# Optimization experiments

Hardware: AMD Instinct MI355X
Metric: run time of the kernel (lower is better)

## Reference

```python
import jax, jax.numpy as jnp
import numpy as np

N = 50000   # nodes
E = 800000  # edges (avg degree 16)
D = 256     # input = hidden = output dim
L = 3       # num_layers


def setup_inputs() -> dict:
    key = jax.random.key(0)
    k0, k1, k2, k3 = jax.random.split(key, 4)
    x = jax.random.normal(k0, (N, D), dtype=jnp.float32)
    edge_index = jax.random.randint(k1, (2, E), 0, N, dtype=jnp.int32)
    # SAGEConv params per layer: lin_l (neighbor path, with bias), lin_r (root path)
    Wl = jax.random.normal(k2, (L, D, D), dtype=jnp.float32) * 0.05
    Wr = jax.random.normal(k3, (L, D, D), dtype=jnp.float32) * 0.05
    b = jnp.zeros((L, D), dtype=jnp.float32)
    return {"x": x, "edge_index": edge_index, "Wl": Wl, "Wr": Wr, "b": b}


def reference(x, edge_index, Wl, Wr, b):
    src = edge_index[0]
    dst = edge_index[1]
    # in-degree for mean aggregation (clamped to avoid div-by-zero)
    deg = jax.ops.segment_sum(jnp.ones((E,), x.dtype), dst, num_segments=N)
    inv_deg = (1.0 / jnp.maximum(deg, 1.0))[:, None]  # [N,1]
    h = x
    for i in range(L):
        # gather source features, scatter-add into destinations, then mean
        agg = jax.ops.segment_sum(h[src], dst, num_segments=N) * inv_deg  # [N,D]
        h = agg @ Wl[i] + h @ Wr[i] + b[i]
        if i < L - 1:
            h = jax.nn.relu(h)  # dropout(p=0.1) is identity in eval mode
    return h
```

## Files before the change

kernel.cpp:

```cpp
#include <hip/hip_runtime.h>


typedef __attribute__((ext_vector_type(8))) _Float16 f16x8;
typedef __attribute__((ext_vector_type(4))) float f32x4;

__global__ void count_deg_kernel(const int* __restrict__ dst,
                                 int* __restrict__ deg, int E) {
    int e = blockIdx.x * blockDim.x + threadIdx.x;
    if (e < E) atomicAdd(&deg[dst[e]], 1);
}

__device__ __forceinline__ int block_excl_scan_256(int v, int tid) {
    int lane = tid & 63, w = tid >> 6;
    int x = v;
#pragma unroll
    for (int off = 1; off < 64; off <<= 1) {
        int y = __shfl_up(x, off);
        if (lane >= off) x += y;
    }
    __shared__ int wsum[4], woff[4];
    if (lane == 63) wsum[w] = x;
    __syncthreads();
    if (tid == 0) {
        int a = 0;
#pragma unroll
        for (int i = 0; i < 4; ++i) { woff[i] = a; a += wsum[i]; }
    }
    __syncthreads();
    return woff[w] + x - v;
}

__global__ void scan_phase1(const int* __restrict__ deg,
                            int* __restrict__ partial, int n) {
    int base = blockIdx.x * 1024;
    int s = 0;
    for (int i = threadIdx.x; i < 1024; i += 256) {
        int idx = base + i;
        s += (idx < n) ? deg[idx] : 0;
    }
    __shared__ int ws4[4];
    int lane = threadIdx.x & 63, w = threadIdx.x >> 6;
#pragma unroll
    for (int off = 32; off; off >>= 1) s += __shfl_down(s, off);
    if (lane == 0) ws4[w] = s;
    __syncthreads();
    if (threadIdx.x == 0)
        partial[blockIdx.x] = ws4[0] + ws4[1] + ws4[2] + ws4[3];
}

__global__ void scan_phase2(int* __restrict__ partial, int nb,
                            int* __restrict__ rowptr, int n, int E) {
    int tid = threadIdx.x;
    int v = (tid < nb) ? partial[tid] : 0;
    int ex = block_excl_scan_256(v, tid);
    if (tid < nb) partial[tid] = ex;
    if (tid == 0) rowptr[n] = E;
}

__global__ void scan_phase3(const int* __restrict__ deg,
                            const int* __restrict__ partial,
                            int* __restrict__ rowptr, int* __restrict__ cursor,
                            float* __restrict__ inv_deg, int n) {
    int base = blockIdx.x * 1024 + threadIdx.x * 4;
    int d[4];
#pragma unroll
    for (int j = 0; j < 4; ++j) {
        int idx = base + j;
        d[j] = (idx < n) ? deg[idx] : 0;
    }
    int tsum = d[0] + d[1] + d[2] + d[3];
    int ex = block_excl_scan_256(tsum, threadIdx.x);
    int run = partial[blockIdx.x] + ex;
#pragma unroll
    for (int j = 0; j < 4; ++j) {
        int idx = base + j;
        if (idx < n) {
            rowptr[idx] = run;
            cursor[idx] = run;
            inv_deg[idx] = 1.0f / (float)max(d[j], 1);
        }
        run += d[j];
    }
}

__global__ void fill_csr_kernel(const int* __restrict__ src,
                                const int* __restrict__ dst,
                                int* __restrict__ cursor,
                                int* __restrict__ csr_src, int E) {
    int e = blockIdx.x * blockDim.x + threadIdx.x;
    if (e < E) {
        int d = dst[e];
        int pos = atomicAdd(&cursor[d], 1);
        csr_src[pos] = src[e];
    }
}

__global__ void presplit_w_kernel(const float* __restrict__ Wl,
                                  const float* __restrict__ Wr,
                                  _Float16* __restrict__ Wf, int total) {
    int idx = blockIdx.x * blockDim.x + threadIdx.x;
    if (idx >= total) return;
    int l = idx >> 17;
    int rem = idx & 131071;
    int s = rem >> 16;
    int kc = rem & 65535;
    int k = kc >> 8, c = kc & 255;
    const float* W = s ? Wr : Wl;
    float w = W[((size_t)l * 256 + k) * 256 + c];
    int k0c = k >> 5, g = (k >> 3) & 3, j = k & 7;
    int tile = c >> 4, col = c & 15;
    int fi = (l * 2 + s) * 65536 + k0c * 8192 + ((tile * 4 + g) * 16 + col) * 8 + j;
    Wf[fi] = (_Float16)w;
}

__device__ __forceinline__ void gemm_from_lds64(
    const _Float16 (*Ah)[65][8], int tid, const _Float16* __restrict__ Wf_l,
    const float* __restrict__ bias, _Float16* __restrict__ zl,
    _Float16* __restrict__ zr, int r0, int M) {
    const int wave = tid >> 6, lane = tid & 63;
    const int l15 = lane & 15, lg = lane >> 4;
    const int wr = (wave & 1) * 32;
    const int wc = (wave >> 1) * 64;

    f32x4 accl[2][4], accr[2][4];
#pragma unroll
    for (int rt = 0; rt < 2; ++rt)
#pragma unroll
        for (int t = 0; t < 4; ++t) {
            accl[rt][t] = (f32x4)(0.0f);
            accr[rt][t] = (f32x4)(0.0f);
        }

#pragma unroll
    for (int k0 = 0; k0 < 256; k0 += 32) {
        f16x8 a0 = *(const f16x8*)&Ah[(k0 >> 3) + lg][wr + l15][0];
        f16x8 a1 = *(const f16x8*)&Ah[(k0 >> 3) + lg][wr + 16 + l15][0];
        const _Float16* wb = Wf_l + (k0 >> 5) * 8192 + (lg * 16 + l15) * 8;
#pragma unroll
        for (int t = 0; t < 4; ++t) {
            int tg = (wc >> 4) + t;
            f16x8 bl = *(const f16x8*)&wb[tg * 512];
            f16x8 br = *(const f16x8*)&wb[65536 + tg * 512];
            accl[0][t] = __builtin_amdgcn_mfma_f32_16x16x32_f16(a0, bl,
                                                                accl[0][t], 0, 0, 0);
            accl[1][t] = __builtin_amdgcn_mfma_f32_16x16x32_f16(a1, bl,
                                                                accl[1][t], 0, 0, 0);
            accr[0][t] = __builtin_amdgcn_mfma_f32_16x16x32_f16(a0, br,
                                                                accr[0][t], 0, 0, 0);
            accr[1][t] = __builtin_amdgcn_mfma_f32_16x16x32_f16(a1, br,
                                                                accr[1][t], 0, 0, 0);
        }
    }

    float bv[4];
#pragma unroll
    for (int t = 0; t < 4; ++t) bv[t] = bias[wc + t * 16 + l15];
#pragma unroll
    for (int rt = 0; rt < 2; ++rt) {
#pragma unroll
        for (int r = 0; r < 4; ++r) {
            int grow = r0 + wr + rt * 16 + lg * 4 + r;
            if (grow >= M) continue;
#pragma unroll
            for (int t = 0; t < 4; ++t) {
                int col = wc + t * 16 + l15;
                zl[(size_t)grow * 256 + col] = (_Float16)accl[rt][t][r];
                zr[(size_t)grow * 256 + col] =
                    (_Float16)(accr[rt][t][r] + bv[t]);
            }
        }
    }
}

__device__ __forceinline__ void gemm_from_lds32(
    const _Float16 (*Ah)[33][8], int tid, const _Float16* __restrict__ Wf_l,
    const float* __restrict__ bias, _Float16* __restrict__ zl,
    _Float16* __restrict__ zr, int r0, int M) {
    const int wave = tid >> 6, lane = tid & 63;
    const int l15 = lane & 15, lg = lane >> 4;
    const int wr = (wave & 1) * 16;
    const int wc = (wave >> 1) * 64;

    f32x4 accl[4], accr[4];
#pragma unroll
    for (int t = 0; t < 4; ++t) {
        accl[t] = (f32x4)(0.0f);
        accr[t] = (f32x4)(0.0f);
    }

#pragma unroll
    for (int k0 = 0; k0 < 256; k0 += 32) {
        f16x8 a = *(const f16x8*)&Ah[(k0 >> 3) + lg][wr + l15][0];
        const _Float16* wb = Wf_l + (k0 >> 5) * 8192 + (lg * 16 + l15) * 8;
#pragma unroll
        for (int t = 0; t < 4; ++t) {
            int tg = (wc >> 4) + t;
            f16x8 bl = *(const f16x8*)&wb[tg * 512];
            f16x8 br = *(const f16x8*)&wb[65536 + tg * 512];
            accl[t] = __builtin_amdgcn_mfma_f32_16x16x32_f16(a, bl, accl[t],
                                                             0, 0, 0);
            accr[t] = __builtin_amdgcn_mfma_f32_16x16x32_f16(a, br, accr[t],
                                                             0, 0, 0);
        }
    }

    float bv[4];
#pragma unroll
    for (int t = 0; t < 4; ++t) bv[t] = bias[wc + t * 16 + l15];
#pragma unroll
    for (int r = 0; r < 4; ++r) {
        int grow = r0 + wr + lg * 4 + r;
        if (grow >= M) continue;
#pragma unroll
        for (int t = 0; t < 4; ++t) {
            int col = wc + t * 16 + l15;
            zl[(size_t)grow * 256 + col] = (_Float16)accl[t][r];
            zr[(size_t)grow * 256 + col] = (_Float16)(accr[t][r] + bv[t]);
        }
    }
}

__global__ __launch_bounds__(512) void gemm0_kernel(
    const float* __restrict__ xsrc, _Float16* __restrict__ zl,
    _Float16* __restrict__ zr, const _Float16* __restrict__ Wf_l,
    const float* __restrict__ bias, int M) {
    __shared__ __align__(16) _Float16 Ah[32][65][8];
    const int tid = threadIdx.x;
    const int r0 = blockIdx.x * 64;
#pragma unroll
    for (int i = 0; i < 4; ++i) {
        int idx = i * 512 + tid;
        int row = idx >> 5, g = idx & 31;
        int grow = r0 + row;
        f16x8 v = (f16x8)(_Float16)0;
        if (grow < M) {
            const float4* p = (const float4*)&xsrc[(size_t)grow * 256 + g * 8];
            float4 v0 = p[0], v1 = p[1];
            v[0] = (_Float16)v0.x; v[1] = (_Float16)v0.y;
            v[2] = (_Float16)v0.z; v[3] = (_Float16)v0.w;
            v[4] = (_Float16)v1.x; v[5] = (_Float16)v1.y;
            v[6] = (_Float16)v1.z; v[7] = (_Float16)v1.w;
        }
        *(f16x8*)&Ah[g][row][0] = v;
    }
    __syncthreads();
    gemm_from_lds64(Ah, tid, Wf_l, bias, zl, zr, r0, M);
}

__global__ __launch_bounds__(512) void fused_layer_kernel(
    const _Float16* __restrict__ zl_in, const _Float16* __restrict__ zr_in,
    _Float16* __restrict__ zl_out, _Float16* __restrict__ zr_out,
    const int* __restrict__ rowptr, const int* __restrict__ csr_src,
    const float* __restrict__ inv_deg, const _Float16* __restrict__ Wf_l,
    const float* __restrict__ bias, int M) {
    __shared__ __align__(16) _Float16 Ah[32][33][8];
    const int tid = threadIdx.x;
    const int hw = tid >> 5, li = tid & 31;
    const int r0 = blockIdx.x * 32;

#pragma unroll
    for (int i = 0; i < 2; ++i) {
        int row = hw * 2 + i;
        int v = r0 + row;
        f16x8 hv = (f16x8)(_Float16)0;
        if (v < M) {
            int beg = rowptr[v], end = rowptr[v + 1];
            float acc[8] = {0.f, 0.f, 0.f, 0.f, 0.f, 0.f, 0.f, 0.f};
            for (int e = beg; e < end; e += 8) {
                f16x8 t[8];
#pragma unroll
                for (int k = 0; k < 8; ++k) {
                    int ee = min(e + k, end - 1);
                    int u = csr_src[ee];
                    t[k] = *(const f16x8*)&zl_in[(size_t)u * 256 + li * 8];
                }
#pragma unroll
                for (int k = 0; k < 8; ++k) {
                    if (e + k < end) {
#pragma unroll
                        for (int j = 0; j < 8; ++j) acc[j] += (float)t[k][j];
                    }
                }
            }
            float sc = inv_deg[v];
            f16x8 zp = *(const f16x8*)&zr_in[(size_t)v * 256 + li * 8];
#pragma unroll
            for (int j = 0; j < 8; ++j)
                hv[j] = (_Float16)fmaxf(acc[j] * sc + (float)zp[j], 0.0f);
        }
        *(f16x8*)&Ah[li][row][0] = hv;
    }
    __syncthreads();
    gemm_from_lds32(Ah, tid, Wf_l, bias, zl_out, zr_out, r0, M);
}

__global__ void combine_final_kernel(const _Float16* __restrict__ zl,
                                     const _Float16* __restrict__ zr,
                                     const int* __restrict__ rowptr,
                                     const int* __restrict__ csr_src,
                                     const float* __restrict__ inv_deg,
                                     float* __restrict__ fout, int n) {
    int hw = threadIdx.x >> 5, li = threadIdx.x & 31;
    int v = blockIdx.x * 8 + hw;
    if (v >= n) return;
    int beg = rowptr[v], end = rowptr[v + 1];
    float acc[8] = {0.f, 0.f, 0.f, 0.f, 0.f, 0.f, 0.f, 0.f};
    for (int e = beg; e < end; e += 8) {
        f16x8 t[8];
#pragma unroll
        for (int k = 0; k < 8; ++k) {
            int ee = min(e + k, end - 1);
            int u = csr_src[ee];
            t[k] = *(const f16x8*)&zl[(size_t)u * 256 + li * 8];
        }
#pragma unroll
        for (int k = 0; k < 8; ++k) {
            if (e + k < end) {
#pragma unroll
                for (int j = 0; j < 8; ++j) acc[j] += (float)t[k][j];
            }
        }
    }
    float sc = inv_deg[v];
    f16x8 zp = *(const f16x8*)&zr[(size_t)v * 256 + li * 8];
    float o[8];
#pragma unroll
    for (int j = 0; j < 8; ++j) o[j] = acc[j] * sc + (float)zp[j];
    float4* op = (float4*)&fout[(size_t)v * 256 + li * 8];
    op[0] = make_float4(o[0], o[1], o[2], o[3]);
    op[1] = make_float4(o[4], o[5], o[6], o[7]);
}

extern "C" void kernel_launch(void* const* d_in, const int* in_sizes, int n_in,
                              void* d_out, int out_size, void* d_ws, size_t ws_size,
                              hipStream_t stream) {
    const int D = 256;
    const int N = in_sizes[0] / D;
    const int E = in_sizes[1] / 2;
    const int L = in_sizes[2] / (D * D);

    const float* x  = (const float*)d_in[0];
    const int*   ei = (const int*)d_in[1];
    const float* Wl = (const float*)d_in[2];
    const float* Wr = (const float*)d_in[3];
    const float* b  = (const float*)d_in[4];
    const int* src = ei;
    const int* dst = ei + E;

    size_t off = 0;
    auto alloc = [&](size_t bytes) {
        void* p = (char*)d_ws + off;
        off += (bytes + 255) & ~(size_t)255;
        return p;
    };
    int*   deg     = (int*)alloc((size_t)N * 4);
    int*   rowptr  = (int*)alloc((size_t)(N + 1) * 4);
    int*   cursor  = (int*)alloc((size_t)N * 4);
    float* inv_deg = (float*)alloc((size_t)N * 4);
    int*   csr_src = (int*)alloc((size_t)E * 4);
    int*   partial = (int*)alloc(256 * 4);
    _Float16* zlA = (_Float16*)alloc((size_t)N * D * 2);
    _Float16* zrA = (_Float16*)alloc((size_t)N * D * 2);
    _Float16* Wf  = (_Float16*)alloc((size_t)L * 2 * 65536 * 2);
    (void)ws_size;

    _Float16* zlB = (_Float16*)d_out;
    _Float16* zrB = zlB + (size_t)N * D;
    float* outf = (float*)d_out;

    const int scan_blocks = (N + 1023) / 1024;

    hipMemsetAsync(deg, 0, (size_t)N * 4, stream);
    hipLaunchKernelGGL(count_deg_kernel, dim3((E + 255) / 256), dim3(256), 0,
                       stream, dst, deg, E);
    hipLaunchKernelGGL(scan_phase1, dim3(scan_blocks), dim3(256), 0, stream,
                       deg, partial, N);
    hipLaunchKernelGGL(scan_phase2, dim3(1), dim3(256), 0, stream,
                       partial, scan_blocks, rowptr, N, E);
    hipLaunchKernelGGL(scan_phase3, dim3(scan_blocks), dim3(256), 0, stream,
                       deg, partial, rowptr, cursor, inv_deg, N);
    hipLaunchKernelGGL(fill_csr_kernel, dim3((E + 255) / 256), dim3(256), 0,
                       stream, src, dst, cursor, csr_src, E);

    int wtotal = L * 2 * 65536;
    hipLaunchKernelGGL(presplit_w_kernel, dim3((wtotal + 255) / 256), dim3(256),
                       0, stream, Wl, Wr, Wf, wtotal);

    const int gemm0_blocks = (N + 63) / 64;
    const int fused_blocks = (N + 31) / 32;
    const int comb_blocks = (N + 7) / 8;

    hipLaunchKernelGGL(gemm0_kernel, dim3(gemm0_blocks), dim3(512), 0, stream,
                       x, zlA, zrA, Wf, b, N);
    hipLaunchKernelGGL(fused_layer_kernel, dim3(fused_blocks), dim3(512), 0,
                       stream, zlA, zrA, zlB, zrB, rowptr, csr_src, inv_deg,
                       Wf + 131072, b + D, N);
    hipLaunchKernelGGL(fused_layer_kernel, dim3(fused_blocks), dim3(512), 0,
                       stream, zlB, zrB, zlA, zrA, rowptr, csr_src, inv_deg,
                       Wf + 262144, b + 2 * D, N);
    hipLaunchKernelGGL(combine_final_kernel, dim3(comb_blocks), dim3(256), 0,
                       stream, zlA, zrA, rowptr, csr_src, inv_deg, outf, N);
}
```

Before: 389.6 us.

## Widen fused layer tiles, prefetch weights, merge memset, vectorize CSR build

The fused aggregation+GEMM layer now handles 64 rows per block instead of 32 and reuses the 64-row GEMM routine, so each block reads the weights once for twice as many rows. The GEMM inner loop now loads the next K-slice of weights into registers while the current slice's MFMAs run. The degree memset is folded into the weight presplit kernel, which now launches first. Degree counting and CSR fill each handle two edges per thread with int2 loads. The 64-row tile halves the number of blocks in the gather-heavy layers, which may reduce latency hiding, and the register double buffer raises register pressure.

```diff
diff --git a/kernel.cpp b/kernel.cpp
--- a/kernel.cpp
+++ b/kernel.cpp
@@ -6,8 +6,14 @@
 
 __global__ void count_deg_kernel(const int* __restrict__ dst,
                                  int* __restrict__ deg, int E) {
-    int e = blockIdx.x * blockDim.x + threadIdx.x;
-    if (e < E) atomicAdd(&deg[dst[e]], 1);
+    int i = (blockIdx.x * blockDim.x + threadIdx.x) * 2;
+    if (i + 1 < E) {
+        int2 d = *(const int2*)&dst[i];
+        atomicAdd(&deg[d.x], 1);
+        atomicAdd(&deg[d.y], 1);
+    } else if (i < E) {
+        atomicAdd(&deg[dst[i]], 1);
+    }
 }
 
 __device__ __forceinline__ int block_excl_scan_256(int v, int tid) {
@@ -87,18 +93,26 @@
                                 const int* __restrict__ dst,
                                 int* __restrict__ cursor,
                                 int* __restrict__ csr_src, int E) {
-    int e = blockIdx.x * blockDim.x + threadIdx.x;
-    if (e < E) {
-        int d = dst[e];
-        int pos = atomicAdd(&cursor[d], 1);
-        csr_src[pos] = src[e];
+    int i = (blockIdx.x * blockDim.x + threadIdx.x) * 2;
+    if (i + 1 < E) {
+        int2 d = *(const int2*)&dst[i];
+        int2 s = *(const int2*)&src[i];
+        int p0 = atomicAdd(&cursor[d.x], 1);
+        csr_src[p0] = s.x;
+        int p1 = atomicAdd(&cursor[d.y], 1);
+        csr_src[p1] = s.y;
+    } else if (i < E) {
+        int p = atomicAdd(&cursor[dst[i]], 1);
+        csr_src[p] = src[i];
     }
 }
 
 __global__ void presplit_w_kernel(const float* __restrict__ Wl,
                                   const float* __restrict__ Wr,
-                                  _Float16* __restrict__ Wf, int total) {
+                                  _Float16* __restrict__ Wf,
+                                  int* __restrict__ deg, int N, int total) {
     int idx = blockIdx.x * blockDim.x + threadIdx.x;
+    if (idx < N) deg[idx] = 0;
     if (idx >= total) return;
     int l = idx >> 17;
     int rem = idx & 131071;
@@ -121,6 +135,8 @@
     const int l15 = lane & 15, lg = lane >> 4;
     const int wr = (wave & 1) * 32;
     const int wc = (wave >> 1) * 64;
+    const int tg0 = wc >> 4;
+    const _Float16* wbase = Wf_l + (lg * 16 + l15) * 8;
 
     f32x4 accl[2][4], accr[2][4];
 #pragma unroll
@@ -131,24 +147,43 @@
             accr[rt][t] = (f32x4)(0.0f);
         }
 
-#pragma unroll
-    for (int k0 = 0; k0 < 256; k0 += 32) {
-        f16x8 a0 = *(const f16x8*)&Ah[(k0 >> 3) + lg][wr + l15][0];
-        f16x8 a1 = *(const f16x8*)&Ah[(k0 >> 3) + lg][wr + 16 + l15][0];
-        const _Float16* wb = Wf_l + (k0 >> 5) * 8192 + (lg * 16 + l15) * 8;
+    f16x8 blc[4], brc[4];
+#pragma unroll
+    for (int t = 0; t < 4; ++t) {
+        blc[t] = *(const f16x8*)&wbase[(tg0 + t) * 512];
+        brc[t] = *(const f16x8*)&wbase[65536 + (tg0 + t) * 512];
+    }
+
+#pragma unroll
+    for (int s = 0; s < 8; ++s) {
+        f16x8 bln[4], brn[4];
+        if (s < 7) {
+            const _Float16* wn = wbase + (s + 1) * 8192;
+#pragma unroll
+            for (int t = 0; t < 4; ++t) {
+                bln[t] = *(const f16x8*)&wn[(tg0 + t) * 512];
+                brn[t] = *(const f16x8*)&wn[65536 + (tg0 + t) * 512];
+            }
+        }
+        f16x8 a0 = *(const f16x8*)&Ah[s * 4 + lg][wr + l15][0];
+        f16x8 a1 = *(const f16x8*)&Ah[s * 4 + lg][wr + 16 + l15][0];
 #pragma unroll
         for (int t = 0; t < 4; ++t) {
-            int tg = (wc >> 4) + t;
-            f16x8 bl = *(const f16x8*)&wb[tg * 512];
-            f16x8 br = *(const f16x8*)&wb[65536 + tg * 512];
-            accl[0][t] = __builtin_amdgcn_mfma_f32_16x16x32_f16(a0, bl,
+            accl[0][t] = __builtin_amdgcn_mfma_f32_16x16x32_f16(a0, blc[t],
                                                                 accl[0][t], 0, 0, 0);
-            accl[1][t] = __builtin_amdgcn_mfma_f32_16x16x32_f16(a1, bl,
+            accl[1][t] = __builtin_amdgcn_mfma_f32_16x16x32_f16(a1, blc[t],
                                                                 accl[1][t], 0, 0, 0);
-            accr[0][t] = __builtin_amdgcn_mfma_f32_16x16x32_f16(a0, br,
+            accr[0][t] = __builtin_amdgcn_mfma_f32_16x16x32_f16(a0, brc[t],
                                                                 accr[0][t], 0, 0, 0);
-            accr[1][t] = __builtin_amdgcn_mfma_f32_16x16x32_f16(a1, br,
+            accr[1][t] = __builtin_amdgcn_mfma_f32_16x16x32_f16(a1, brc[t],
                                                                 accr[1][t], 0, 0, 0);
+        }
+        if (s < 7) {
+#pragma unroll
+            for (int t = 0; t < 4; ++t) {
+                blc[t] = bln[t];
+                brc[t] = brn[t];
+            }
         }
     }
 
@@ -168,54 +203,6 @@
                 zr[(size_t)grow * 256 + col] =
                     (_Float16)(accr[rt][t][r] + bv[t]);
             }
-        }
-    }
-}
-
-__device__ __forceinline__ void gemm_from_lds32(
-    const _Float16 (*Ah)[33][8], int tid, const _Float16* __restrict__ Wf_l,
-    const float* __restrict__ bias, _Float16* __restrict__ zl,
-    _Float16* __restrict__ zr, int r0, int M) {
-    const int wave = tid >> 6, lane = tid & 63;
-    const int l15 = lane & 15, lg = lane >> 4;
-    const int wr = (wave & 1) * 16;
-    const int wc = (wave >> 1) * 64;
-
-    f32x4 accl[4], accr[4];
-#pragma unroll
-    for (int t = 0; t < 4; ++t) {
-        accl[t] = (f32x4)(0.0f);
-        accr[t] = (f32x4)(0.0f);
-    }
-
-#pragma unroll
-    for (int k0 = 0; k0 < 256; k0 += 32) {
-        f16x8 a = *(const f16x8*)&Ah[(k0 >> 3) + lg][wr + l15][0];
-        const _Float16* wb = Wf_l + (k0 >> 5) * 8192 + (lg * 16 + l15) * 8;
-#pragma unroll
-        for (int t = 0; t < 4; ++t) {
-            int tg = (wc >> 4) + t;
-            f16x8 bl = *(const f16x8*)&wb[tg * 512];
-            f16x8 br = *(const f16x8*)&wb[65536 + tg * 512];
-            accl[t] = __builtin_amdgcn_mfma_f32_16x16x32_f16(a, bl, accl[t],
-                                                             0, 0, 0);
-            accr[t] = __builtin_amdgcn_mfma_f32_16x16x32_f16(a, br, accr[t],
-                                                             0, 0, 0);
-        }
-    }
-
-    float bv[4];
-#pragma unroll
-    for (int t = 0; t < 4; ++t) bv[t] = bias[wc + t * 16 + l15];
-#pragma unroll
-    for (int r = 0; r < 4; ++r) {
-        int grow = r0 + wr + lg * 4 + r;
-        if (grow >= M) continue;
-#pragma unroll
-        for (int t = 0; t < 4; ++t) {
-            int col = wc + t * 16 + l15;
-            zl[(size_t)grow * 256 + col] = (_Float16)accl[t][r];
-            zr[(size_t)grow * 256 + col] = (_Float16)(accr[t][r] + bv[t]);
         }
     }
 }
@@ -253,18 +240,20 @@
     const int* __restrict__ rowptr, const int* __restrict__ csr_src,
     const float* __restrict__ inv_deg, const _Float16* __restrict__ Wf_l,
     const float* __restrict__ bias, int M) {
-    __shared__ __align__(16) _Float16 Ah[32][33][8];
+    __shared__ __align__(16) _Float16 Ah[32][65][8];
     const int tid = threadIdx.x;
     const int hw = tid >> 5, li = tid & 31;
-    const int r0 = blockIdx.x * 32;
-
-#pragma unroll
-    for (int i = 0; i < 2; ++i) {
-        int row = hw * 2 + i;
+    const int r0 = blockIdx.x * 64;
+
+#pragma unroll
+    for (int i = 0; i < 4; ++i) {
+        int row = hw * 4 + i;
         int v = r0 + row;
         f16x8 hv = (f16x8)(_Float16)0;
         if (v < M) {
             int beg = rowptr[v], end = rowptr[v + 1];
+            float sc = inv_deg[v];
+            f16x8 zp = *(const f16x8*)&zr_in[(size_t)v * 256 + li * 8];
             float acc[8] = {0.f, 0.f, 0.f, 0.f, 0.f, 0.f, 0.f, 0.f};
             for (int e = beg; e < end; e += 8) {
                 f16x8 t[8];
@@ -282,8 +271,6 @@
                     }
                 }
             }
-            float sc = inv_deg[v];
-            f16x8 zp = *(const f16x8*)&zr_in[(size_t)v * 256 + li * 8];
 #pragma unroll
             for (int j = 0; j < 8; ++j)
                 hv[j] = (_Float16)fmaxf(acc[j] * sc + (float)zp[j], 0.0f);
@@ -291,7 +278,7 @@
         *(f16x8*)&Ah[li][row][0] = hv;
     }
     __syncthreads();
-    gemm_from_lds32(Ah, tid, Wf_l, bias, zl_out, zr_out, r0, M);
+    gemm_from_lds64(Ah, tid, Wf_l, bias, zl_out, zr_out, r0, M);
 }
 
 __global__ void combine_final_kernel(const _Float16* __restrict__ zl,
@@ -370,32 +357,30 @@
 
     const int scan_blocks = (N + 1023) / 1024;
 
-    hipMemsetAsync(deg, 0, (size_t)N * 4, stream);
-    hipLaunchKernelGGL(count_deg_kernel, dim3((E + 255) / 256), dim3(256), 0,
-                       stream, dst, deg, E);
+    int wtotal = L * 2 * 65536;
+    hipLaunchKernelGGL(presplit_w_kernel, dim3((wtotal + 255) / 256), dim3(256),
+                       0, stream, Wl, Wr, Wf, deg, N, wtotal);
+
+    hipLaunchKernelGGL(count_deg_kernel, dim3((E / 2 + 255) / 256), dim3(256),
+                       0, stream, dst, deg, E);
     hipLaunchKernelGGL(scan_phase1, dim3(scan_blocks), dim3(256), 0, stream,
                        deg, partial, N);
     hipLaunchKernelGGL(scan_phase2, dim3(1), dim3(256), 0, stream,
                        partial, scan_blocks, rowptr, N, E);
     hipLaunchKernelGGL(scan_phase3, dim3(scan_blocks), dim3(256), 0, stream,
                        deg, partial, rowptr, cursor, inv_deg, N);
-    hipLaunchKernelGGL(fill_csr_kernel, dim3((E + 255) / 256), dim3(256), 0,
-                       stream, src, dst, cursor, csr_src, E);
-
-    int wtotal = L * 2 * 65536;
-    hipLaunchKernelGGL(presplit_w_kernel, dim3((wtotal + 255) / 256), dim3(256),
-                       0, stream, Wl, Wr, Wf, wtotal);
-
-    const int gemm0_blocks = (N + 63) / 64;
-    const int fused_blocks = (N + 31) / 32;
+    hipLaunchKernelGGL(fill_csr_kernel, dim3((E / 2 + 255) / 256), dim3(256),
+                       0, stream, src, dst, cursor, csr_src, E);
+
+    const int gemm_blocks = (N + 63) / 64;
     const int comb_blocks = (N + 7) / 8;
 
-    hipLaunchKernelGGL(gemm0_kernel, dim3(gemm0_blocks), dim3(512), 0, stream,
+    hipLaunchKernelGGL(gemm0_kernel, dim3(gemm_blocks), dim3(512), 0, stream,
                        x, zlA, zrA, Wf, b, N);
-    hipLaunchKernelGGL(fused_layer_kernel, dim3(fused_blocks), dim3(512), 0,
+    hipLaunchKernelGGL(fused_layer_kernel, dim3(gemm_blocks), dim3(512), 0,
                        stream, zlA, zrA, zlB, zrB, rowptr, csr_src, inv_deg,
                        Wf + 131072, b + D, N);
-    hipLaunchKernelGGL(fused_layer_kernel, dim3(fused_blocks), dim3(512), 0,
+    hipLaunchKernelGGL(fused_layer_kernel, dim3(gemm_blocks), dim3(512), 0,
                        stream, zlB, zrB, zlA, zrA, rowptr, csr_src, inv_deg,
                        Wf + 262144, b + 2 * D, N);
     hipLaunchKernelGGL(combine_final_kernel, dim3(comb_blocks), dim3(256), 0,
```

New measurement: 370.6 us. 4.9% less time.
